# Optimization experiments

Measured on AMD Instinct MI355X. Metric: run time of the kernel, lower is better.

Reference implementation:

```python
import jax, jax.numpy as jnp
import numpy as np

N = 100000
E = 1600000
IN_DIM = 32
LATENT = 64
K = 3          # num_hops
L = 5          # num_layers


def setup_inputs() -> dict:
    key = jax.random.key(0)
    ks = jax.random.split(key, 8)
    x = jax.random.normal(ks[0], (N, IN_DIM), dtype=jnp.float32)
    edge_index = jax.random.randint(ks[1], (2, E), 0, N, dtype=jnp.int64)
    edge_weight = jax.random.uniform(ks[2], (E,), dtype=jnp.float32)
    # TAGConv params: per layer, (K+1) hop-wise linear weights + one bias
    s0 = 1.0 / np.sqrt(IN_DIM)
    s1 = 1.0 / np.sqrt(LATENT)
    W0 = jax.random.uniform(ks[3], (K + 1, IN_DIM, LATENT), jnp.float32, -s0, s0)
    b0 = jnp.zeros((LATENT,), jnp.float32)
    Ws = jax.random.uniform(ks[4], (L - 1, K + 1, LATENT, LATENT), jnp.float32, -s1, s1)
    bs = jnp.zeros((L - 1, LATENT), jnp.float32)
    return {"x": x, "edge_index": edge_index, "edge_weight": edge_weight,
            "W0": W0, "b0": b0, "Ws": Ws, "bs": bs}


def _gcn_norm(edge_index, edge_weight, num_nodes):
    # TAGConv uses gcn_norm with add_self_loops=False (symmetric normalization)
    row, col = edge_index[0], edge_index[1]
    deg = jax.ops.segment_sum(edge_weight, col, num_segments=num_nodes)
    safe = jnp.where(deg > 0, deg, 1.0)
    dinv = jnp.where(deg > 0, 1.0 / jnp.sqrt(safe), 0.0)
    return dinv[row] * edge_weight * dinv[col]


def _tagconv(x, row, col, norm, W, b, num_nodes):
    # out = sum_{k=0}^{K} (A_hat^k x) @ W[k] + b
    out = x @ W[0]
    h = x
    for k in range(1, W.shape[0]):
        h = jax.ops.segment_sum(norm[:, None] * h[row], col, num_segments=num_nodes)
        out = out + h @ W[k]
    return out + b


def reference(x, edge_index, edge_weight, W0, b0, Ws, bs):
    row, col = edge_index[0], edge_index[1]
    norm = _gcn_norm(edge_index, edge_weight, N)
    h = jax.nn.relu(_tagconv(x, row, col, norm, W0, b0, N))
    for i in range(Ws.shape[0]):
        h = jax.nn.relu(_tagconv(h, row, col, norm, Ws[i], bs[i], N))
    return h
```

## Files before the change

kernel.cpp:

```cpp
#include <hip/hip_runtime.h>
#include <hip/hip_fp16.h>

#define NN 100000
#define NE 1600000
#define NBKT 196
#define BSH 9
#define BCAP 9216
#define NCOL (NBKT * 512)
#define EPB_A 4096

typedef __half half_t;
using f16x8 = __attribute__((ext_vector_type(8))) _Float16;
using f32x4 = __attribute__((ext_vector_type(4))) float;


__device__ inline float4 load4(const float* p) {
    return *reinterpret_cast<const float4*>(p);
}
__device__ inline float4 load4(const half_t* p) {
    uint2 u = *reinterpret_cast<const uint2*>(p);
    __half2 a = *reinterpret_cast<__half2*>(&u.x);
    __half2 b = *reinterpret_cast<__half2*>(&u.y);
    float2 fa = __half22float2(a), fb = __half22float2(b);
    return make_float4(fa.x, fa.y, fb.x, fb.y);
}
__device__ inline void store_half4(half_t* p, float4 v) {
    __half2 a = __floats2half2_rn(v.x, v.y);
    __half2 b = __floats2half2_rn(v.z, v.w);
    uint2 u;
    u.x = *reinterpret_cast<unsigned*>(&a);
    u.y = *reinterpret_cast<unsigned*>(&b);
    *reinterpret_cast<uint2*>(p) = u;
}


__global__ void f32_to_f16(const float* __restrict__ in, half_t* __restrict__ out, int nquad) {
    int i = blockIdx.x * blockDim.x + threadIdx.x;
    if (i < nquad) store_half4(out + i * 4, load4(in + i * 4));
}

__global__ __launch_bounds__(256) void passA_bucket(
    const int* __restrict__ row, const int* __restrict__ col, const float* __restrict__ w,
    unsigned* __restrict__ gcur, int2* __restrict__ gbkt, int E)
{
    __shared__ unsigned cnt[256];
    __shared__ unsigned lofs[256];
    __shared__ unsigned lcur[256];
    __shared__ unsigned gb[256];
    __shared__ int2 arena[EPB_A];
    __shared__ unsigned short abkt[EPB_A];
    int t = threadIdx.x;
    int base = blockIdx.x * EPB_A;
    int nloc = min(EPB_A, E - base);
    cnt[t] = 0; lcur[t] = 0;
    __syncthreads();
    for (int i = t; i < nloc; i += 256)
        atomicAdd(&cnt[col[base + i] >> BSH], 1u);
    __syncthreads();
    unsigned v = cnt[t];
    lofs[t] = v; __syncthreads();
    for (int d = 1; d < 256; d <<= 1) {
        unsigned u = (t >= d) ? lofs[t - d] : 0u;
        __syncthreads();
        lofs[t] += u;
        __syncthreads();
    }
    unsigned excl = lofs[t] - v;
    __syncthreads();
    lofs[t] = excl;
    __syncthreads();
    if (t < NBKT && cnt[t] > 0) gb[t] = atomicAdd(&gcur[t], cnt[t]);
    for (int i = t; i < nloc; i += 256) {
        int e = base + i;
        int c = col[e];
        int b = c >> BSH;
        unsigned p = lofs[b] + atomicAdd(&lcur[b], 1u);
        unsigned packed = ((unsigned)(c & 511) << 17) | (unsigned)row[e];
        arena[p] = make_int2((int)packed, __float_as_int(w[e]));
        abkt[p] = (unsigned short)b;
    }
    __syncthreads();
    for (int i = t; i < nloc; i += 256) {
        int b = abkt[i];
        unsigned j = i - lofs[b];
        gbkt[(size_t)b * BCAP + gb[b] + j] = arena[i];
    }
}

__global__ __launch_bounds__(256) void passB_hist(
    const int2* __restrict__ gbkt, const unsigned* __restrict__ gcur,
    unsigned* __restrict__ cnt, float* __restrict__ deg)
{
    __shared__ unsigned c512[512];
    __shared__ float d512[512];
    int t = threadIdx.x;
    int b = blockIdx.x;
    for (int i = t; i < 512; i += 256) { c512[i] = 0; d512[i] = 0.f; }
    __syncthreads();
    unsigned sz = min(gcur[b], (unsigned)BCAP);
    const int2* src = gbkt + (size_t)b * BCAP;
    for (unsigned i = t; i < sz; i += 256) {
        int2 v = src[i];
        unsigned colw = ((unsigned)v.x) >> 17;
        atomicAdd(&c512[colw], 1u);
        atomicAdd(&d512[colw], __int_as_float(v.y));
    }
    __syncthreads();
    for (int i = t; i < 512; i += 256) {
        cnt[b * 512 + i] = c512[i];
        deg[b * 512 + i] = d512[i];
    }
}

__global__ void dinv_kernel(const float* __restrict__ deg, float* __restrict__ dinv, int n) {
    int i = blockIdx.x * blockDim.x + threadIdx.x;
    if (i < n) {
        float d = deg[i];
        dinv[i] = d > 0.f ? rsqrtf(d) : 0.f;
    }
}

__global__ void scan_phase1(const unsigned* __restrict__ cnt, unsigned* __restrict__ bsum, int n) {
    __shared__ unsigned sh[256];
    int t = threadIdx.x;
    int base = blockIdx.x * 1024 + t * 4;
    unsigned s = 0;
#pragma unroll
    for (int j = 0; j < 4; j++) { int i = base + j; if (i < n) s += cnt[i]; }
    sh[t] = s; __syncthreads();
    for (int d = 128; d > 0; d >>= 1) {
        if (t < d) sh[t] += sh[t + d];
        __syncthreads();
    }
    if (t == 0) bsum[blockIdx.x] = sh[0];
}

__global__ void scan_phase2(const unsigned* __restrict__ bsum, unsigned* __restrict__ bbase, int nb) {
    __shared__ unsigned sh[128];
    int t = threadIdx.x;
    unsigned v = (t < nb) ? bsum[t] : 0u;
    sh[t] = v; __syncthreads();
    for (int d = 1; d < 128; d <<= 1) {
        unsigned u = (t >= d) ? sh[t - d] : 0u;
        __syncthreads();
        sh[t] += u;
        __syncthreads();
    }
    if (t < nb) bbase[t] = sh[t] - v;
}

__global__ void scan_phase3(const unsigned* __restrict__ cnt, const unsigned* __restrict__ bbase,
                            unsigned* __restrict__ offsets, int n) {
    __shared__ unsigned sh[256];
    int t = threadIdx.x;
    int base = blockIdx.x * 1024 + t * 4;
    unsigned c[4]; unsigned s = 0;
#pragma unroll
    for (int j = 0; j < 4; j++) { int i = base + j; c[j] = (i < n) ? cnt[i] : 0u; s += c[j]; }
    sh[t] = s; __syncthreads();
    for (int d = 1; d < 256; d <<= 1) {
        unsigned u = (t >= d) ? sh[t - d] : 0u;
        __syncthreads();
        sh[t] += u;
        __syncthreads();
    }
    unsigned o = bbase[blockIdx.x] + sh[t] - s;
#pragma unroll
    for (int j = 0; j < 4; j++) {
        int i = base + j;
        if (i < n) { offsets[i] = o; o += c[j]; }
    }
}

__global__ __launch_bounds__(256) void passC_place(
    const int2* __restrict__ gbkt, const unsigned* __restrict__ gcur,
    const unsigned* __restrict__ offsets, const float* __restrict__ dinv,
    int2* __restrict__ ent)
{
    __shared__ unsigned lcur[512];
    int t = threadIdx.x;
    int b = blockIdx.x;
    for (int i = t; i < 512; i += 256) lcur[i] = 0;
    __syncthreads();
    unsigned sz = min(gcur[b], (unsigned)BCAP);
    const int2* src = gbkt + (size_t)b * BCAP;
    for (unsigned i = t; i < sz; i += 256) {
        int2 v = src[i];
        unsigned colw = ((unsigned)v.x) >> 17;
        int r = v.x & 0x1FFFF;
        int c = (b << BSH) | (int)colw;
        unsigned pos = offsets[c] + atomicAdd(&lcur[colw], 1u);
        float wv = __int_as_float(v.y) * dinv[r];
        ent[pos] = make_int2(r, __float_as_int(wv));
    }
}


__global__ __launch_bounds__(256) void spmm32_kernel(
    const half_t* __restrict__ src, half_t* __restrict__ pout,
    const int2* __restrict__ ent, const unsigned* __restrict__ offs,
    const unsigned* __restrict__ cnt, const float* __restrict__ dinv, int n)
{
    int node = blockIdx.x * 32 + (threadIdx.x >> 3);
    int f = (threadIdx.x & 7) * 4;
    if (node >= n) return;
    unsigned e = offs[node];
    unsigned end = e + cnt[node];
    float dv = dinv[node];
    float acc[4] = {};
    for (; e + 8 <= end; e += 8) {
        int2 en[8];
#pragma unroll
        for (int j = 0; j < 8; ++j) en[j] = ent[e + j];
        uint2 raw[8];
#pragma unroll
        for (int j = 0; j < 8; ++j)
            raw[j] = *reinterpret_cast<const uint2*>(src + (size_t)en[j].x * 32 + f);
#pragma unroll
        for (int j = 0; j < 8; ++j) {
            float w = __int_as_float(en[j].y);
            __half2* h2 = reinterpret_cast<__half2*>(&raw[j]);
            float2 v0 = __half22float2(h2[0]), v1 = __half22float2(h2[1]);
            acc[0] += w * v0.x; acc[1] += w * v0.y;
            acc[2] += w * v1.x; acc[3] += w * v1.y;
        }
    }
    for (; e < end; ++e) {
        int2 en = ent[e];
        float w = __int_as_float(en.y);
        uint2 raw = *reinterpret_cast<const uint2*>(src + (size_t)en.x * 32 + f);
        __half2* h2 = reinterpret_cast<__half2*>(&raw);
        float2 v0 = __half22float2(h2[0]), v1 = __half22float2(h2[1]);
        acc[0] += w * v0.x; acc[1] += w * v0.y;
        acc[2] += w * v1.x; acc[3] += w * v1.y;
    }
    uint2 o;
    __half2 h;
    h = __floats2half2_rn(acc[0] * dv, acc[1] * dv); o.x = *reinterpret_cast<unsigned*>(&h);
    h = __floats2half2_rn(acc[2] * dv, acc[3] * dv); o.y = *reinterpret_cast<unsigned*>(&h);
    *reinterpret_cast<uint2*>(pout + (size_t)node * 32 + f) = o;
}


__global__ __launch_bounds__(256) void spmm64_kernel(
    const half_t* __restrict__ src, half_t* __restrict__ pout,
    const int2* __restrict__ ent, const unsigned* __restrict__ offs,
    const unsigned* __restrict__ cnt, const float* __restrict__ dinv, int n)
{
    int node = blockIdx.x * 32 + (threadIdx.x >> 3);
    int f = (threadIdx.x & 7) * 8;
    if (node >= n) return;
    unsigned e = offs[node];
    unsigned end = e + cnt[node];
    float dv = dinv[node];
    float acc[8] = {};
    for (; e + 8 <= end; e += 8) {
        int2 en[8];
#pragma unroll
        for (int j = 0; j < 8; ++j) en[j] = ent[e + j];
        uint4 raw[8];
#pragma unroll
        for (int j = 0; j < 8; ++j)
            raw[j] = *reinterpret_cast<const uint4*>(src + (size_t)en[j].x * 64 + f);
#pragma unroll
        for (int j = 0; j < 8; ++j) {
            float w = __int_as_float(en[j].y);
            __half2* h2 = reinterpret_cast<__half2*>(&raw[j]);
#pragma unroll
            for (int q = 0; q < 4; ++q) {
                float2 v = __half22float2(h2[q]);
                acc[2 * q]     += w * v.x;
                acc[2 * q + 1] += w * v.y;
            }
        }
    }
    for (; e < end; ++e) {
        int2 en = ent[e];
        float w = __int_as_float(en.y);
        uint4 raw = *reinterpret_cast<const uint4*>(src + (size_t)en.x * 64 + f);
        __half2* h2 = reinterpret_cast<__half2*>(&raw);
#pragma unroll
        for (int q = 0; q < 4; ++q) {
            float2 v = __half22float2(h2[q]);
            acc[2 * q]     += w * v.x;
            acc[2 * q + 1] += w * v.y;
        }
    }
    uint4 o;
    __half2 h;
    h = __floats2half2_rn(acc[0] * dv, acc[1] * dv); o.x = *reinterpret_cast<unsigned*>(&h);
    h = __floats2half2_rn(acc[2] * dv, acc[3] * dv); o.y = *reinterpret_cast<unsigned*>(&h);
    h = __floats2half2_rn(acc[4] * dv, acc[5] * dv); o.z = *reinterpret_cast<unsigned*>(&h);
    h = __floats2half2_rn(acc[6] * dv, acc[7] * dv); o.w = *reinterpret_cast<unsigned*>(&h);
    *reinterpret_cast<uint4*>(pout + (size_t)node * 64 + f) = o;
}


template <int IN, int MODE>
__global__ __launch_bounds__(256) void fused4_mfma(
    const half_t* __restrict__ A0, const half_t* __restrict__ P1,
    const half_t* __restrict__ P2, const half_t* __restrict__ P3,
    const float* __restrict__ W, const float* __restrict__ bias,
    half_t* __restrict__ hdst, float* __restrict__ fdst, int n)
{
    constexpr int KK  = IN / 32;
    constexpr int WTS = IN + 8;
    __shared__ _Float16 Wt[64][WTS];
    int t = threadIdx.x;
    int w = t >> 6, l = t & 63;
    int nodeBase = blockIdx.x * 64;
    int rowTop = nodeBase + w * 16;

    f32x4 acc[4];
#pragma unroll
    for (int ct = 0; ct < 4; ++ct) acc[ct] = (f32x4){0.f, 0.f, 0.f, 0.f};

    int row = rowTop + (l & 15);
    if (row >= n) row = n - 1;
    const int khome = (l >> 4) * 8;

#pragma unroll
    for (int s = 0; s < 4; ++s) {
        const half_t* S = (s == 0) ? A0 : (s == 1) ? P1 : (s == 2) ? P2 : P3;
        const float* Wsrc = W + s * IN * 64;
        for (int idx = t; idx < IN * 64; idx += 256) {
            int k = idx >> 6, colj = idx & 63;
            Wt[colj][k] = (_Float16)Wsrc[idx];
        }
        __syncthreads();
#pragma unroll
        for (int kk = 0; kk < KK; ++kk) {
            uint4 araw = *reinterpret_cast<const uint4*>(S + (size_t)row * IN + kk * 32 + khome);
            f16x8 afrag = __builtin_bit_cast(f16x8, araw);
#pragma unroll
            for (int ct = 0; ct < 4; ++ct) {
                f16x8 bfrag = *reinterpret_cast<const f16x8*>(&Wt[ct * 16 + (l & 15)][kk * 32 + khome]);
                acc[ct] = __builtin_amdgcn_mfma_f32_16x16x32_f16(afrag, bfrag, acc[ct], 0, 0, 0);
            }
        }
        __syncthreads();
    }

    int colb = l & 15;
    int rbase = rowTop + (l >> 4) * 4;
#pragma unroll
    for (int ct = 0; ct < 4; ++ct) {
#pragma unroll
        for (int r = 0; r < 4; ++r) {
            int node = rbase + r;
            if (node >= n) continue;
            int colj = ct * 16 + colb;
            float v = fmaxf(acc[ct][r] + bias[colj], 0.f);
            size_t o = (size_t)node * 64 + colj;
            if (MODE == 1) hdst[o] = __float2half_rn(v);
            else           fdst[o] = v;
        }
    }
}


extern "C" void kernel_launch(void* const* d_in, const int* in_sizes, int n_in,
                              void* d_out, int out_size, void* d_ws, size_t ws_size,
                              hipStream_t stream) {
    const float* x  = (const float*)d_in[0];
    const int*   ei = (const int*)d_in[1];
    const float* ew = (const float*)d_in[2];
    const float* W0 = (const float*)d_in[3];
    const float* b0 = (const float*)d_in[4];
    const float* Ws = (const float*)d_in[5];
    const float* bs = (const float*)d_in[6];
    float* out = (float*)d_out;

    const int* row = ei;
    const int* col = ei + NE;

    char* wsp = (char*)d_ws;
    auto alloc = [&](size_t bytes) -> char* {
        char* p = wsp;
        wsp += (bytes + 255) & ~(size_t)255;
        return p;
    };
    float*    dinv    = (float*)alloc((size_t)NCOL * 4);
    float*    deg     = (float*)alloc((size_t)NCOL * 4);
    unsigned* cnt     = (unsigned*)alloc((size_t)NCOL * 4);
    unsigned* offsets = (unsigned*)alloc((size_t)NCOL * 4);
    unsigned* bsum    = (unsigned*)alloc(256 * 4);
    unsigned* bbase   = (unsigned*)alloc(256 * 4);
    unsigned* gcur    = (unsigned*)alloc(NBKT * 4);
    int2*     ent     = (int2*)alloc((size_t)NE * 8);
    half_t*   xh      = (half_t*)alloc((size_t)NN * 32 * 2);
    half_t*   B0      = (half_t*)alloc((size_t)NN * 64 * 2);
    half_t*   P1      = (half_t*)alloc((size_t)NN * 64 * 2);
    half_t*   P2      = (half_t*)alloc((size_t)NN * 64 * 2);
    half_t*   P3      = (half_t*)alloc((size_t)NN * 64 * 2);
    int2*     gbkt    = (int2*)P1;

    hipMemsetAsync(gcur, 0, NBKT * 4, stream);

    f32_to_f16<<<(NN * 32 / 4 + 255) / 256, 256, 0, stream>>>(x, xh, NN * 32 / 4);

    const int AB = (NE + EPB_A - 1) / EPB_A;
    passA_bucket<<<AB, 256, 0, stream>>>(row, col, ew, gcur, gbkt, NE);
    passB_hist<<<NBKT, 256, 0, stream>>>(gbkt, gcur, cnt, deg);
    dinv_kernel<<<(NN + 255) / 256, 256, 0, stream>>>(deg, dinv, NN);
    const int NB = NCOL / 1024;
    scan_phase1<<<NB, 256, 0, stream>>>(cnt, bsum, NCOL);
    scan_phase2<<<1, 128, 0, stream>>>(bsum, bbase, NB);
    scan_phase3<<<NB, 256, 0, stream>>>(cnt, bbase, offsets, NCOL);
    passC_place<<<NBKT, 256, 0, stream>>>(gbkt, gcur, offsets, dinv, ent);

    const int MMB = (NN + 63) / 64;
    const int SB  = (NN + 31) / 32;

    spmm32_kernel<<<SB, 256, 0, stream>>>(xh, P1, ent, offsets, cnt, dinv, NN);
    spmm32_kernel<<<SB, 256, 0, stream>>>(P1, P2, ent, offsets, cnt, dinv, NN);
    spmm32_kernel<<<SB, 256, 0, stream>>>(P2, P3, ent, offsets, cnt, dinv, NN);
    fused4_mfma<32, 1><<<MMB, 256, 0, stream>>>(xh, P1, P2, P3, W0, b0, B0, nullptr, NN);

    for (int l = 0; l < 4; ++l) {
        const float* Wl = Ws + (size_t)l * 4 * 64 * 64;
        const float* bl = bs + (size_t)l * 64;
        spmm64_kernel<<<SB, 256, 0, stream>>>(B0, P1, ent, offsets, cnt, dinv, NN);
        spmm64_kernel<<<SB, 256, 0, stream>>>(P1, P2, ent, offsets, cnt, dinv, NN);
        spmm64_kernel<<<SB, 256, 0, stream>>>(P2, P3, ent, offsets, cnt, dinv, NN);
        if (l < 3)
            fused4_mfma<64, 1><<<MMB, 256, 0, stream>>>(B0, P1, P2, P3, Wl, bl, B0, nullptr, NN);
        else
            fused4_mfma<64, 2><<<MMB, 256, 0, stream>>>(B0, P1, P2, P3, Wl, bl, nullptr, out, NN);
    }
}
```

Baseline: 735.4 us.

## Pack CSR edge entries into 32-bit row index plus fp16 weight

Edge entries shrink from an int2 (row, fp32 weight) to one 32-bit word holding a 17-bit row index and a 15-bit fp16 weight with the sign bit dropped, which is valid because the weights are non-negative. This halves the edge-stream bandwidth in every SpMM pass and in the placement kernel. The SpMM inner loops also drop the manual 8-way batched gather in favour of a simple loop with unroll 2, which may reduce memory-level parallelism. Weight precision falls to fp16.

```diff
diff --git a/kernel.cpp b/kernel.cpp
--- a/kernel.cpp
+++ b/kernel.cpp
@@ -31,6 +31,11 @@
     u.x = *reinterpret_cast<unsigned*>(&a);
     u.y = *reinterpret_cast<unsigned*>(&b);
     *reinterpret_cast<uint2*>(p) = u;
+}
+__device__ inline void edec(unsigned p, int& r, float& w) {
+    r = (int)(p >> 15);
+    unsigned short hb = (unsigned short)(p & 0x7FFFu);
+    w = __half2float(*reinterpret_cast<__half*>(&hb));
 }
 
 
@@ -175,7 +180,7 @@
 __global__ __launch_bounds__(256) void passC_place(
     const int2* __restrict__ gbkt, const unsigned* __restrict__ gcur,
     const unsigned* __restrict__ offsets, const float* __restrict__ dinv,
-    int2* __restrict__ ent)
+    unsigned* __restrict__ ent)
 {
     __shared__ unsigned lcur[512];
     int t = threadIdx.x;
@@ -191,44 +196,30 @@
         int c = (b << BSH) | (int)colw;
         unsigned pos = offsets[c] + atomicAdd(&lcur[colw], 1u);
         float wv = __int_as_float(v.y) * dinv[r];
-        ent[pos] = make_int2(r, __float_as_int(wv));
+        __half hh = __float2half_rn(wv);
+        unsigned hb = *reinterpret_cast<unsigned short*>(&hh);
+        ent[pos] = ((unsigned)r << 15) | hb;
     }
 }
 
 
 __global__ __launch_bounds__(256) void spmm32_kernel(
     const half_t* __restrict__ src, half_t* __restrict__ pout,
-    const int2* __restrict__ ent, const unsigned* __restrict__ offs,
+    const unsigned* __restrict__ ent, const unsigned* __restrict__ offs,
     const unsigned* __restrict__ cnt, const float* __restrict__ dinv, int n)
 {
     int node = blockIdx.x * 32 + (threadIdx.x >> 3);
     int f = (threadIdx.x & 7) * 4;
     if (node >= n) return;
-    unsigned e = offs[node];
-    unsigned end = e + cnt[node];
+    unsigned off = offs[node];
+    unsigned c = cnt[node];
     float dv = dinv[node];
     float acc[4] = {};
-    for (; e + 8 <= end; e += 8) {
-        int2 en[8];
-#pragma unroll
-        for (int j = 0; j < 8; ++j) en[j] = ent[e + j];
-        uint2 raw[8];
-#pragma unroll
-        for (int j = 0; j < 8; ++j)
-            raw[j] = *reinterpret_cast<const uint2*>(src + (size_t)en[j].x * 32 + f);
-#pragma unroll
-        for (int j = 0; j < 8; ++j) {
-            float w = __int_as_float(en[j].y);
-            __half2* h2 = reinterpret_cast<__half2*>(&raw[j]);
-            float2 v0 = __half22float2(h2[0]), v1 = __half22float2(h2[1]);
-            acc[0] += w * v0.x; acc[1] += w * v0.y;
-            acc[2] += w * v1.x; acc[3] += w * v1.y;
-        }
-    }
-    for (; e < end; ++e) {
-        int2 en = ent[e];
-        float w = __int_as_float(en.y);
-        uint2 raw = *reinterpret_cast<const uint2*>(src + (size_t)en.x * 32 + f);
+#pragma unroll 2
+    for (unsigned e = off; e < off + c; ++e) {
+        int r; float w;
+        edec(ent[e], r, w);
+        uint2 raw = *reinterpret_cast<const uint2*>(src + (size_t)r * 32 + f);
         __half2* h2 = reinterpret_cast<__half2*>(&raw);
         float2 v0 = __half22float2(h2[0]), v1 = __half22float2(h2[1]);
         acc[0] += w * v0.x; acc[1] += w * v0.y;
@@ -244,40 +235,20 @@
 
 __global__ __launch_bounds__(256) void spmm64_kernel(
     const half_t* __restrict__ src, half_t* __restrict__ pout,
-    const int2* __restrict__ ent, const unsigned* __restrict__ offs,
+    const unsigned* __restrict__ ent, const unsigned* __restrict__ offs,
     const unsigned* __restrict__ cnt, const float* __restrict__ dinv, int n)
 {
     int node = blockIdx.x * 32 + (threadIdx.x >> 3);
     int f = (threadIdx.x & 7) * 8;
     if (node >= n) return;
-    unsigned e = offs[node];
-    unsigned end = e + cnt[node];
+    unsigned off = offs[node], c = cnt[node];
     float dv = dinv[node];
     float acc[8] = {};
-    for (; e + 8 <= end; e += 8) {
-        int2 en[8];
-#pragma unroll
-        for (int j = 0; j < 8; ++j) en[j] = ent[e + j];
-        uint4 raw[8];
-#pragma unroll
-        for (int j = 0; j < 8; ++j)
-            raw[j] = *reinterpret_cast<const uint4*>(src + (size_t)en[j].x * 64 + f);
-#pragma unroll
-        for (int j = 0; j < 8; ++j) {
-            float w = __int_as_float(en[j].y);
-            __half2* h2 = reinterpret_cast<__half2*>(&raw[j]);
-#pragma unroll
-            for (int q = 0; q < 4; ++q) {
-                float2 v = __half22float2(h2[q]);
-                acc[2 * q]     += w * v.x;
-                acc[2 * q + 1] += w * v.y;
-            }
-        }
-    }
-    for (; e < end; ++e) {
-        int2 en = ent[e];
-        float w = __int_as_float(en.y);
-        uint4 raw = *reinterpret_cast<const uint4*>(src + (size_t)en.x * 64 + f);
+#pragma unroll 2
+    for (unsigned e = off; e < off + c; ++e) {
+        int r; float w;
+        edec(ent[e], r, w);
+        uint4 raw = *reinterpret_cast<const uint4*>(src + (size_t)r * 64 + f);
         __half2* h2 = reinterpret_cast<__half2*>(&raw);
 #pragma unroll
         for (int q = 0; q < 4; ++q) {
@@ -387,7 +358,7 @@
     unsigned* bsum    = (unsigned*)alloc(256 * 4);
     unsigned* bbase   = (unsigned*)alloc(256 * 4);
     unsigned* gcur    = (unsigned*)alloc(NBKT * 4);
-    int2*     ent     = (int2*)alloc((size_t)NE * 8);
+    unsigned* ent     = (unsigned*)alloc((size_t)NE * 4);
     half_t*   xh      = (half_t*)alloc((size_t)NN * 32 * 2);
     half_t*   B0      = (half_t*)alloc((size_t)NN * 64 * 2);
     half_t*   P1      = (half_t*)alloc((size_t)NN * 64 * 2);
```

Result: faster. 633.1 us (-13.9%).
